# Kernel tuning notes

Hardware: AMD Instinct MI355X
Metric: run time of the kernel (lower is better)

## Reference

```python
import jax, jax.numpy as jnp
import numpy as np

N_NODES = 50000
N_EDGES = 800000
N_GRAPHS = 256
W_SCALE = 0.05  # keep activations bounded through 5 relu conv layers


def setup_inputs() -> dict:
    key = jax.random.key(0)
    ks = jax.random.split(key, 16)
    rn = lambda k, shape: W_SCALE * jax.random.normal(k, shape, dtype=jnp.float32)
    return {
        "x": jax.random.normal(ks[0], (N_NODES, 336), dtype=jnp.float32),
        "edge_index": jax.random.randint(ks[1], (2, N_EDGES), 0, N_NODES, dtype=jnp.int32),
        "batch": jnp.sort(jax.random.randint(ks[2], (N_NODES,), 0, N_GRAPHS, dtype=jnp.int32)),
        "w1_rel": rn(ks[3], (100, 336)),
        "w1_root": rn(ks[4], (100, 336)),
        "b1": rn(ks[5], (100,)),
        "w_rel": rn(ks[6], (4, 100, 100)),
        "w_root": rn(ks[7], (4, 100, 100)),
        "b": rn(ks[8], (4, 100)),
        "lw1": rn(ks[9], (100, 100)),
        "lb1": rn(ks[10], (100,)),
        "lw2": rn(ks[11], (100, 100)),
        "lb2": rn(ks[12], (100,)),
        "lw3": rn(ks[13], (29, 100)),
        "lb3": rn(ks[14], (29,)),
    }


def _graph_conv(x, edge_index, w_rel, w_root, bias):
    # PyG GraphConv: out_i = W_rel @ (sum_{j->i} x_j) + b + W_root @ x_i
    src, dst = edge_index[0], edge_index[1]
    agg = jax.ops.segment_sum(x[src], dst, num_segments=x.shape[0])  # [N, d_in]
    return agg @ w_rel.T + bias + x @ w_root.T


def reference(x, edge_index, batch, w1_rel, w1_root, b1, w_rel, w_root, b,
              lw1, lb1, lw2, lb2, lw3, lb3):
    h = jax.nn.relu(_graph_conv(x, edge_index, w1_rel, w1_root, b1))  # [N,100]
    for i in range(4):  # conv2..conv5 (structurally distinct params)
        h = jax.nn.relu(_graph_conv(h, edge_index, w_rel[i], w_root[i], b[i]))
    # global_mean_pool over graphs
    sums = jax.ops.segment_sum(h, batch, num_segments=N_GRAPHS)          # [G,100]
    counts = jax.ops.segment_sum(jnp.ones((h.shape[0],), h.dtype), batch,
                                 num_segments=N_GRAPHS)                  # [G]
    pooled = sums / jnp.maximum(counts, 1.0)[:, None]
    h = jax.nn.relu(pooled @ lw1.T + lb1)
    h = jax.nn.relu(h @ lw2.T + lb2)
    return h @ lw3.T + lb3  # [G, 29]
```

## Files before the change

kernel.cpp:

```cpp
#include <hip/hip_runtime.h>

#define N_NODES 50000
#define N_EDGES 800000
#define N_GRAPHS 256
#define F 100

#define SCAN_B 512
#define SCAN_NB 98
#define SCAN_PAD (SCAN_NB * SCAN_B)

typedef __attribute__((ext_vector_type(8))) short bf16x8;
typedef __attribute__((ext_vector_type(4))) float f32x4;
typedef unsigned short ushort_t;
typedef unsigned int uint_t;

__device__ inline ushort_t f2bf(float f) {
  uint_t u = __float_as_uint(f);
  uint_t r = (u + 0x7fffu + ((u >> 16) & 1u)) >> 16;
  return (ushort_t)r;
}


__global__ void hist_kernel(const int* __restrict__ dst, int* __restrict__ cnt, int E) {
  int e = blockIdx.x * blockDim.x + threadIdx.x;
  if (e < E) atomicAdd(&cnt[dst[e]], 1);
}

__global__ __launch_bounds__(SCAN_B) void scan1_kernel(const int* __restrict__ cnt,
                                                       int* __restrict__ excl,
                                                       int* __restrict__ bsum) {
  __shared__ int sh[SCAN_B];
  int t = threadIdx.x;
  int i = blockIdx.x * SCAN_B + t;
  int v = cnt[i];
  sh[t] = v;
  __syncthreads();
  for (int off = 1; off < SCAN_B; off <<= 1) {
    int u = (t >= off) ? sh[t - off] : 0;
    __syncthreads();
    sh[t] += u;
    __syncthreads();
  }
  excl[i] = sh[t] - v;
  if (t == SCAN_B - 1) bsum[blockIdx.x] = sh[t];
}

__global__ __launch_bounds__(128) void scan2_kernel(int* __restrict__ bsum) {
  __shared__ int sh[128];
  int t = threadIdx.x;
  int v = (t < SCAN_NB) ? bsum[t] : 0;
  sh[t] = v;
  __syncthreads();
  for (int off = 1; off < 128; off <<= 1) {
    int u = (t >= off) ? sh[t - off] : 0;
    __syncthreads();
    sh[t] += u;
    __syncthreads();
  }
  if (t < SCAN_NB) bsum[t] = sh[t] - v;
}

__global__ __launch_bounds__(SCAN_B) void scan3_kernel(const int* __restrict__ excl,
                                                       const int* __restrict__ bsum,
                                                       int* __restrict__ offs,
                                                       int* __restrict__ cursor) {
  int i = blockIdx.x * SCAN_B + threadIdx.x;
  int v = excl[i] + bsum[blockIdx.x];
  if (i <= N_NODES) { offs[i] = v; cursor[i] = v; }
}

__global__ void fill_kernel(const int* __restrict__ src, const int* __restrict__ dst,
                            int* __restrict__ cursor, int* __restrict__ csr_src, int E) {
  int e = blockIdx.x * blockDim.x + threadIdx.x;
  if (e < E) {
    int p = atomicAdd(&cursor[dst[e]], 1);
    csr_src[p] = src[e];
  }
}


__global__ void pack_w1_kernel(const float* __restrict__ w1_rel, const float* __restrict__ w1_root,
                               ushort_t* __restrict__ Wp1) {
  int row = blockIdx.x;
  for (int k = threadIdx.x; k < 352; k += 128) {
    float v = 0.f;
    if (k < 336) {
      if (row < 100) v = w1_rel[row * 336 + k];
      else if (row < 200) v = w1_root[(row - 100) * 336 + k];
    }
    Wp1[(size_t)row * 352 + k] = f2bf(v);
  }
}

__global__ void pack_w_kernel(const float* __restrict__ w_rel, const float* __restrict__ w_root,
                              ushort_t* __restrict__ Wp) {
  int row = blockIdx.x;
  int l = blockIdx.y;
  int k = threadIdx.x;
  float v = 0.f;
  if (k < 100) {
    if (row < 100) v = w_rel[((size_t)l * 100 + row) * 100 + k];
    else if (row < 200) v = w_root[((size_t)l * 100 + row - 100) * 100 + k];
  }
  Wp[((size_t)l * 208 + row) * 128 + k] = f2bf(v);
}


template <bool AF32>
__global__ __launch_bounds__(128) void conv_mfma(
    const void* __restrict__ Aptr, const ushort_t* __restrict__ Wp,
    const float* __restrict__ bias,
    ushort_t* __restrict__ Zrel, ushort_t* __restrict__ Zroot, int Kp) {
  __shared__ short alds[4 * 64 * 8];
  __shared__ short blds[4 * 208 * 8];
  __shared__ float bias_s[100];

  int tid = threadIdx.x;
  int n0 = blockIdx.x * 64;
  if (tid < 100) bias_s[tid] = bias[tid];

  f32x4 acc0[13], acc1[13];
#pragma unroll
  for (int b = 0; b < 13; ++b) { acc0[b] = (f32x4)0.f; acc1[b] = (f32x4)0.f; }

  int w = tid >> 6, lane = tid & 63, q = lane >> 4, m16 = lane & 15;

  for (int k0 = 0; k0 < Kp; k0 += 32) {
#pragma unroll
    for (int i = tid; i < 256; i += 128) {
      int nl = i >> 2, qq = i & 3;
      int node = n0 + nl;
      bf16x8 val = (bf16x8)0;
      if (AF32) {
        int k = k0 + qq * 8;
        if (node < N_NODES && k < 336) {
          const float* p = (const float*)Aptr + (size_t)node * 336 + k;
          float4 f0 = *(const float4*)p;
          float4 f1 = *(const float4*)(p + 4);
          val[0] = (short)f2bf(f0.x); val[1] = (short)f2bf(f0.y);
          val[2] = (short)f2bf(f0.z); val[3] = (short)f2bf(f0.w);
          val[4] = (short)f2bf(f1.x); val[5] = (short)f2bf(f1.y);
          val[6] = (short)f2bf(f1.z); val[7] = (short)f2bf(f1.w);
        }
      } else {
        if (node < N_NODES)
          val = *(const bf16x8*)((const short*)Aptr + (size_t)node * 128 + k0 + qq * 8);
      }
      *(bf16x8*)&alds[(qq * 64 + nl) * 8] = val;
    }
    for (int i = tid; i < 832; i += 128) {
      int n = i >> 2, qq = i & 3;
      *(bf16x8*)&blds[(qq * 208 + n) * 8] =
          *(const bf16x8*)((const short*)Wp + (size_t)n * Kp + k0 + qq * 8);
    }
    __syncthreads();
    bf16x8 a0 = *(const bf16x8*)&alds[(q * 64 + w * 32 + m16) * 8];
    bf16x8 a1 = *(const bf16x8*)&alds[(q * 64 + w * 32 + 16 + m16) * 8];
#pragma unroll
    for (int b = 0; b < 13; ++b) {
      bf16x8 bf = *(const bf16x8*)&blds[(q * 208 + b * 16 + m16) * 8];
      acc0[b] = __builtin_amdgcn_mfma_f32_16x16x32_bf16(a0, bf, acc0[b], 0, 0, 0);
      acc1[b] = __builtin_amdgcn_mfma_f32_16x16x32_bf16(a1, bf, acc1[b], 0, 0, 0);
    }
    __syncthreads();
  }

#pragma unroll
  for (int t = 0; t < 2; ++t) {
    int node_base = n0 + w * 32 + t * 16 + q * 4;
#pragma unroll
    for (int b = 0; b < 13; ++b) {
      int n = b * 16 + m16;
#pragma unroll
      for (int r = 0; r < 4; ++r) {
        int node = node_base + r;
        if (node >= N_NODES) continue;
        float v = t == 0 ? acc0[b][r] : acc1[b][r];
        if (n < 100) {
          Zrel[(size_t)node * 100 + n] = f2bf(v);
        } else if (n < 200) {
          Zroot[(size_t)node * 100 + (n - 100)] = f2bf(v + bias_s[n - 100]);
        }
      }
    }
  }
}


__global__ __launch_bounds__(256) void gather_bf16(
    const ushort_t* __restrict__ Zrel, const ushort_t* __restrict__ Zroot,
    const int* __restrict__ offs, const int* __restrict__ csr,
    ushort_t* __restrict__ H) {
  int node = blockIdx.x * 4 + (threadIdx.x >> 6);
  node = __builtin_amdgcn_readfirstlane(node);
  int lane = threadIdx.x & 63;
  int off = (lane < 50 ? lane : 49) * 2;

  uint_t z = *(const uint_t*)(Zroot + (size_t)node * 100 + off);
  float p0[8], p1[8];
#pragma unroll
  for (int u = 0; u < 8; ++u) { p0[u] = 0.f; p1[u] = 0.f; }
  p0[0] = __uint_as_float(z << 16);
  p1[0] = __uint_as_float(z & 0xffff0000u);

  int s = offs[node], e = offs[node + 1];
  int j = s;
  for (; j + 7 < e; j += 8) {
    uint_t zz[8];
#pragma unroll
    for (int u = 0; u < 8; ++u) {
      int idx = csr[j + u];
      zz[u] = *(const uint_t*)(Zrel + (size_t)idx * 100 + off);
    }
#pragma unroll
    for (int u = 0; u < 8; ++u) {
      p0[u] += __uint_as_float(zz[u] << 16);
      p1[u] += __uint_as_float(zz[u] & 0xffff0000u);
    }
  }
  for (; j < e; ++j) {
    int idx = csr[j];
    uint_t z0 = *(const uint_t*)(Zrel + (size_t)idx * 100 + off);
    p0[0] += __uint_as_float(z0 << 16);
    p1[0] += __uint_as_float(z0 & 0xffff0000u);
  }
  float a0 = ((p0[0] + p0[1]) + (p0[2] + p0[3])) + ((p0[4] + p0[5]) + (p0[6] + p0[7]));
  float a1 = ((p1[0] + p1[1]) + (p1[2] + p1[3])) + ((p1[4] + p1[5]) + (p1[6] + p1[7]));
  a0 = fmaxf(a0, 0.f);
  a1 = fmaxf(a1, 0.f);
  uint_t outp = (uint_t)f2bf(a0) | ((uint_t)f2bf(a1) << 16);
  if (lane >= 50) outp = 0u;
  *(uint_t*)(H + (size_t)node * 128 + lane * 2) = outp;
}


__global__ __launch_bounds__(1024) void pool_kernel(const ushort_t* __restrict__ H,
                                                    const int* __restrict__ batch,
                                                    float* __restrict__ pooled) {
  int g = blockIdx.x;
  int t = threadIdx.x;
  int lo = 0, hi = N_NODES;
  while (lo < hi) { int mid = (lo + hi) >> 1; if (batch[mid] < g) lo = mid + 1; else hi = mid; }
  int s = lo;
  hi = N_NODES;
  while (lo < hi) { int mid = (lo + hi) >> 1; if (batch[mid] <= g) lo = mid + 1; else hi = mid; }
  int e = lo;

  int row = t >> 6;
  int lane = t & 63;
  int off = (lane < 50 ? lane : 49) * 2;
  float a0 = 0.f, a1 = 0.f;
  for (int n = s + row; n < e; n += 16) {
    uint_t z = *(const uint_t*)(H + (size_t)n * 128 + off);
    a0 += __uint_as_float(z << 16);
    a1 += __uint_as_float(z & 0xffff0000u);
  }
  __shared__ float sh[16][104];
  if (lane < 50) { sh[row][lane * 2] = a0; sh[row][lane * 2 + 1] = a1; }
  __syncthreads();
  if (t < 100) {
    float acc = 0.f;
#pragma unroll
    for (int r = 0; r < 16; ++r) acc += sh[r][t];
    int cnt = e - s;
    float d = (cnt > 0) ? (float)cnt : 1.f;
    pooled[(size_t)g * F + t] = acc / d;
  }
}


__global__ void mlp_kernel(const float* __restrict__ pooled,
                           const float* __restrict__ lw1, const float* __restrict__ lb1,
                           const float* __restrict__ lw2, const float* __restrict__ lb2,
                           const float* __restrict__ lw3, const float* __restrict__ lb3,
                           float* __restrict__ out) {
  int g = blockIdx.x;
  int t = threadIdx.x;
  __shared__ float r0[F], r1[F], r2[F];
  if (t < F) r0[t] = pooled[(size_t)g * F + t];
  __syncthreads();
  if (t < F) {
    float s = lb1[t];
    for (int k = 0; k < F; ++k) s += r0[k] * lw1[t * F + k];
    r1[t] = fmaxf(s, 0.f);
  }
  __syncthreads();
  if (t < F) {
    float s = lb2[t];
    for (int k = 0; k < F; ++k) s += r1[k] * lw2[t * F + k];
    r2[t] = fmaxf(s, 0.f);
  }
  __syncthreads();
  if (t < 29) {
    float s = lb3[t];
    for (int k = 0; k < F; ++k) s += r2[k] * lw3[t * F + k];
    out[g * 29 + t] = s;
  }
}


extern "C" void kernel_launch(void* const* d_in, const int* in_sizes, int n_in,
                              void* d_out, int out_size, void* d_ws, size_t ws_size,
                              hipStream_t stream) {
  const float* x       = (const float*)d_in[0];
  const int*   ei      = (const int*)d_in[1];
  const int*   batch   = (const int*)d_in[2];
  const float* w1_rel  = (const float*)d_in[3];
  const float* w1_root = (const float*)d_in[4];
  const float* b1      = (const float*)d_in[5];
  const float* w_rel   = (const float*)d_in[6];
  const float* w_root  = (const float*)d_in[7];
  const float* bvec    = (const float*)d_in[8];
  const float* lw1     = (const float*)d_in[9];
  const float* lb1     = (const float*)d_in[10];
  const float* lw2     = (const float*)d_in[11];
  const float* lb2     = (const float*)d_in[12];
  const float* lw3     = (const float*)d_in[13];
  const float* lb3     = (const float*)d_in[14];
  float* out = (float*)d_out;

  char* ws = (char*)d_ws;
  size_t o = 0;
  auto alloc = [&](size_t bytes) { void* p = ws + o; o = (o + bytes + 511) & ~(size_t)511; return p; };
  ushort_t* H    = (ushort_t*)alloc((size_t)N_NODES * 128 * 2);
  ushort_t* Zrel = (ushort_t*)alloc((size_t)N_NODES * 100 * 2);
  ushort_t* Zroot= (ushort_t*)alloc((size_t)N_NODES * 100 * 2);
  ushort_t* Wp1  = (ushort_t*)alloc((size_t)208 * 352 * 2);
  ushort_t* Wp   = (ushort_t*)alloc((size_t)4 * 208 * 128 * 2);
  float*    pooled = (float*)alloc((size_t)N_GRAPHS * F * 4);
  int* cnt    = (int*)alloc((size_t)SCAN_PAD * 4);
  int* excl   = (int*)alloc((size_t)SCAN_PAD * 4);
  int* bsum   = (int*)alloc((size_t)128 * 4);
  int* offs   = (int*)alloc((size_t)(N_NODES + 1) * 4);
  int* cursor = (int*)alloc((size_t)(N_NODES + 1) * 4);
  int* csr    = (int*)alloc((size_t)N_EDGES * 4);

  const int E = N_EDGES;
  const int* srcv = ei;
  const int* dstv = ei + E;

  hipMemsetAsync(cnt, 0, (size_t)SCAN_PAD * sizeof(int), stream);
  hist_kernel<<<(E + 255) / 256, 256, 0, stream>>>(dstv, cnt, E);
  scan1_kernel<<<SCAN_NB, SCAN_B, 0, stream>>>(cnt, excl, bsum);
  scan2_kernel<<<1, 128, 0, stream>>>(bsum);
  scan3_kernel<<<SCAN_NB, SCAN_B, 0, stream>>>(excl, bsum, offs, cursor);
  fill_kernel<<<(E + 255) / 256, 256, 0, stream>>>(srcv, dstv, cursor, csr, E);

  pack_w1_kernel<<<208, 128, 0, stream>>>(w1_rel, w1_root, Wp1);
  pack_w_kernel<<<dim3(208, 4), 128, 0, stream>>>(w_rel, w_root, Wp);

  int mmgrid = (N_NODES + 63) / 64;
  conv_mfma<true><<<mmgrid, 128, 0, stream>>>(x, Wp1, b1, Zrel, Zroot, 352);
  gather_bf16<<<N_NODES / 4, 256, 0, stream>>>(Zrel, Zroot, offs, csr, H);
  for (int l = 0; l < 4; ++l) {
    conv_mfma<false><<<mmgrid, 128, 0, stream>>>(H, Wp + (size_t)l * 208 * 128,
                                                 bvec + (size_t)l * F, Zrel, Zroot, 128);
    gather_bf16<<<N_NODES / 4, 256, 0, stream>>>(Zrel, Zroot, offs, csr, H);
  }
  pool_kernel<<<N_GRAPHS, 1024, 0, stream>>>(H, batch, pooled);
  mlp_kernel<<<N_GRAPHS, 128, 0, stream>>>(pooled, lw1, lb1, lw2, lb2, lw3, lb3, out);
}
```

Measured before the change: 501.9 us.

## Partition CSR build by destination range and use 4-wave conv tiles

The histogram and fill kernels now give each block one edge chunk and one of eight destination ranges. Each block scans that chunk and counts or places only edges whose destination falls in its range, so atomics hit a narrower address window, at the cost of reading dst eight times. The conv MFMA kernel now runs four waves of 16 rows each instead of two waves of 32. This halves the accumulator registers per thread and raises occupancy, and the LDS layout changes to row-major with 32 shorts per row. Weight tiles are still reloaded per block, and B-fragment reuse per wave is halved.

```diff
diff --git a/kernel.cpp b/kernel.cpp
--- a/kernel.cpp
+++ b/kernel.cpp
@@ -9,6 +9,9 @@
 #define SCAN_NB 98
 #define SCAN_PAD (SCAN_NB * SCAN_B)
 
+#define PART_SZ 6250
+#define FILL_CHUNK 2048
+
 typedef __attribute__((ext_vector_type(8))) short bf16x8;
 typedef __attribute__((ext_vector_type(4))) float f32x4;
 typedef unsigned short ushort_t;
@@ -21,9 +24,16 @@
 }
 
 
-__global__ void hist_kernel(const int* __restrict__ dst, int* __restrict__ cnt, int E) {
-  int e = blockIdx.x * blockDim.x + threadIdx.x;
-  if (e < E) atomicAdd(&cnt[dst[e]], 1);
+__global__ __launch_bounds__(256) void hist_kernel(const int* __restrict__ dst,
+                                                   int* __restrict__ cnt, int E) {
+  int part = blockIdx.x & 7;
+  int lo = part * PART_SZ, hi = lo + PART_SZ;
+  int base = (blockIdx.x >> 3) * FILL_CHUNK;
+  int end = base + FILL_CHUNK; if (end > E) end = E;
+  for (int i = base + threadIdx.x; i < end; i += 256) {
+    int d = dst[i];
+    if (d >= lo && d < hi) atomicAdd(&cnt[d], 1);
+  }
 }
 
 __global__ __launch_bounds__(SCAN_B) void scan1_kernel(const int* __restrict__ cnt,
@@ -69,12 +79,20 @@
   if (i <= N_NODES) { offs[i] = v; cursor[i] = v; }
 }
 
-__global__ void fill_kernel(const int* __restrict__ src, const int* __restrict__ dst,
-                            int* __restrict__ cursor, int* __restrict__ csr_src, int E) {
-  int e = blockIdx.x * blockDim.x + threadIdx.x;
-  if (e < E) {
-    int p = atomicAdd(&cursor[dst[e]], 1);
-    csr_src[p] = src[e];
+__global__ __launch_bounds__(256) void fill_kernel(const int* __restrict__ src,
+                                                   const int* __restrict__ dst,
+                                                   int* __restrict__ cursor,
+                                                   int* __restrict__ csr_src, int E) {
+  int part = blockIdx.x & 7;
+  int lo = part * PART_SZ, hi = lo + PART_SZ;
+  int base = (blockIdx.x >> 3) * FILL_CHUNK;
+  int end = base + FILL_CHUNK; if (end > E) end = E;
+  for (int i = base + threadIdx.x; i < end; i += 256) {
+    int d = dst[i];
+    if (d >= lo && d < hi) {
+      int p = atomicAdd(&cursor[d], 1);
+      csr_src[p] = src[i];
+    }
   }
 }
 
@@ -107,32 +125,31 @@
 
 
 template <bool AF32>
-__global__ __launch_bounds__(128) void conv_mfma(
+__global__ __launch_bounds__(256) void conv_mfma(
     const void* __restrict__ Aptr, const ushort_t* __restrict__ Wp,
     const float* __restrict__ bias,
     ushort_t* __restrict__ Zrel, ushort_t* __restrict__ Zroot, int Kp) {
-  __shared__ short alds[4 * 64 * 8];
-  __shared__ short blds[4 * 208 * 8];
-  __shared__ float bias_s[100];
+  __shared__ short alds[64 * 32];
+  __shared__ short blds[208 * 32];
+  __shared__ float bias_s[104];
 
   int tid = threadIdx.x;
   int n0 = blockIdx.x * 64;
   if (tid < 100) bias_s[tid] = bias[tid];
 
-  f32x4 acc0[13], acc1[13];
-#pragma unroll
-  for (int b = 0; b < 13; ++b) { acc0[b] = (f32x4)0.f; acc1[b] = (f32x4)0.f; }
+  f32x4 acc[13];
+#pragma unroll
+  for (int b = 0; b < 13; ++b) acc[b] = (f32x4)0.f;
 
   int w = tid >> 6, lane = tid & 63, q = lane >> 4, m16 = lane & 15;
 
   for (int k0 = 0; k0 < Kp; k0 += 32) {
-#pragma unroll
-    for (int i = tid; i < 256; i += 128) {
-      int nl = i >> 2, qq = i & 3;
-      int node = n0 + nl;
+    {
+      int r = tid >> 2, qq = tid & 3;
+      int node = n0 + r;
+      int k = k0 + qq * 8;
       bf16x8 val = (bf16x8)0;
       if (AF32) {
-        int k = k0 + qq * 8;
         if (node < N_NODES && k < 336) {
           const float* p = (const float*)Aptr + (size_t)node * 336 + k;
           float4 f0 = *(const float4*)p;
@@ -144,43 +161,38 @@
         }
       } else {
         if (node < N_NODES)
-          val = *(const bf16x8*)((const short*)Aptr + (size_t)node * 128 + k0 + qq * 8);
+          val = *(const bf16x8*)((const short*)Aptr + (size_t)node * 128 + k);
       }
-      *(bf16x8*)&alds[(qq * 64 + nl) * 8] = val;
-    }
-    for (int i = tid; i < 832; i += 128) {
-      int n = i >> 2, qq = i & 3;
-      *(bf16x8*)&blds[(qq * 208 + n) * 8] =
-          *(const bf16x8*)((const short*)Wp + (size_t)n * Kp + k0 + qq * 8);
-    }
-    __syncthreads();
-    bf16x8 a0 = *(const bf16x8*)&alds[(q * 64 + w * 32 + m16) * 8];
-    bf16x8 a1 = *(const bf16x8*)&alds[(q * 64 + w * 32 + 16 + m16) * 8];
+      *(bf16x8*)&alds[r * 32 + qq * 8] = val;
+    }
+    for (int c = tid; c < 832; c += 256) {
+      int r = c >> 2, qq = c & 3;
+      *(bf16x8*)&blds[r * 32 + qq * 8] =
+          *(const bf16x8*)((const short*)Wp + (size_t)r * Kp + k0 + qq * 8);
+    }
+    __syncthreads();
+    bf16x8 a = *(const bf16x8*)&alds[(w * 16 + m16) * 32 + q * 8];
 #pragma unroll
     for (int b = 0; b < 13; ++b) {
-      bf16x8 bf = *(const bf16x8*)&blds[(q * 208 + b * 16 + m16) * 8];
-      acc0[b] = __builtin_amdgcn_mfma_f32_16x16x32_bf16(a0, bf, acc0[b], 0, 0, 0);
-      acc1[b] = __builtin_amdgcn_mfma_f32_16x16x32_bf16(a1, bf, acc1[b], 0, 0, 0);
-    }
-    __syncthreads();
-  }
-
-#pragma unroll
-  for (int t = 0; t < 2; ++t) {
-    int node_base = n0 + w * 32 + t * 16 + q * 4;
-#pragma unroll
-    for (int b = 0; b < 13; ++b) {
-      int n = b * 16 + m16;
-#pragma unroll
-      for (int r = 0; r < 4; ++r) {
-        int node = node_base + r;
-        if (node >= N_NODES) continue;
-        float v = t == 0 ? acc0[b][r] : acc1[b][r];
-        if (n < 100) {
-          Zrel[(size_t)node * 100 + n] = f2bf(v);
-        } else if (n < 200) {
-          Zroot[(size_t)node * 100 + (n - 100)] = f2bf(v + bias_s[n - 100]);
-        }
+      bf16x8 bf = *(const bf16x8*)&blds[(b * 16 + m16) * 32 + q * 8];
+      acc[b] = __builtin_amdgcn_mfma_f32_16x16x32_bf16(a, bf, acc[b], 0, 0, 0);
+    }
+    __syncthreads();
+  }
+
+  int node_base = n0 + w * 16 + q * 4;
+#pragma unroll
+  for (int b = 0; b < 13; ++b) {
+    int n = b * 16 + m16;
+#pragma unroll
+    for (int r = 0; r < 4; ++r) {
+      int node = node_base + r;
+      if (node >= N_NODES) continue;
+      float v = acc[b][r];
+      if (n < 100) {
+        Zrel[(size_t)node * 100 + n] = f2bf(v);
+      } else if (n < 200) {
+        Zroot[(size_t)node * 100 + (n - 100)] = f2bf(v + bias_s[n - 100]);
       }
     }
   }
@@ -339,21 +351,22 @@
   const int* srcv = ei;
   const int* dstv = ei + E;
 
+  int nchunk = (E + FILL_CHUNK - 1) / FILL_CHUNK;
   hipMemsetAsync(cnt, 0, (size_t)SCAN_PAD * sizeof(int), stream);
-  hist_kernel<<<(E + 255) / 256, 256, 0, stream>>>(dstv, cnt, E);
+  hist_kernel<<<nchunk * 8, 256, 0, stream>>>(dstv, cnt, E);
   scan1_kernel<<<SCAN_NB, SCAN_B, 0, stream>>>(cnt, excl, bsum);
   scan2_kernel<<<1, 128, 0, stream>>>(bsum);
   scan3_kernel<<<SCAN_NB, SCAN_B, 0, stream>>>(excl, bsum, offs, cursor);
-  fill_kernel<<<(E + 255) / 256, 256, 0, stream>>>(srcv, dstv, cursor, csr, E);
+  fill_kernel<<<nchunk * 8, 256, 0, stream>>>(srcv, dstv, cursor, csr, E);
 
   pack_w1_kernel<<<208, 128, 0, stream>>>(w1_rel, w1_root, Wp1);
   pack_w_kernel<<<dim3(208, 4), 128, 0, stream>>>(w_rel, w_root, Wp);
 
   int mmgrid = (N_NODES + 63) / 64;
-  conv_mfma<true><<<mmgrid, 128, 0, stream>>>(x, Wp1, b1, Zrel, Zroot, 352);
+  conv_mfma<true><<<mmgrid, 256, 0, stream>>>(x, Wp1, b1, Zrel, Zroot, 352);
   gather_bf16<<<N_NODES / 4, 256, 0, stream>>>(Zrel, Zroot, offs, csr, H);
   for (int l = 0; l < 4; ++l) {
-    conv_mfma<false><<<mmgrid, 128, 0, stream>>>(H, Wp + (size_t)l * 208 * 128,
+    conv_mfma<false><<<mmgrid, 256, 0, stream>>>(H, Wp + (size_t)l * 208 * 128,
                                                  bvec + (size_t)l * F, Zrel, Zroot, 128);
     gather_bf16<<<N_NODES / 4, 256, 0, stream>>>(Zrel, Zroot, offs, csr, H);
   }
```

Result: faster. 475.7 us (-5.2%).
